# Kernel optimization log

Hardware: AMD Instinct MI355X
Metric: run time of the kernel (lower is better)

Reference implementation:

```python
import jax, jax.numpy as jnp
import numpy as np

SIZE = 1024
CODE_DIM = 256
B, H, W = 32, 32, 32


def setup_inputs() -> dict:
    key = jax.random.key(0)
    k1, k2 = jax.random.split(key)
    z = jax.random.normal(k1, (B, CODE_DIM, H, W), dtype=jnp.float32)
    embeddings = jax.random.normal(k2, (SIZE, CODE_DIM), dtype=jnp.float32)
    return {"z": z, "embeddings": embeddings}


def reference(z, embeddings):
    b, c, h, w = z.shape  # c == code_dim
    # (b, h, w, c) -> (N, c)
    flat = jnp.transpose(z, (0, 2, 3, 1)).reshape(-1, c)
    d = (
        jnp.sum(flat * flat, axis=-1, keepdims=True)
        - 2.0 * (flat @ embeddings.T)
        + jnp.sum(embeddings * embeddings, axis=-1)
    )
    idx = jnp.argmin(d, axis=-1)  # (N,)
    quantized = embeddings[idx].reshape(b, h, w, c)
    quantized = jnp.transpose(quantized, (0, 3, 1, 2))  # (b, c, h, w)
    straight_through = jax.lax.stop_gradient(quantized - z) + z
    return quantized, straight_through, idx.reshape(b, h, w)
```

## Files before the change

### kernel.cpp

```cpp
#include <hip/hip_runtime.h>

#define NPTS   32768
#define NCODES 1024
#define DIM    256
#define HWSZ   1024
#define CHW    (DIM*HWSZ)
#define QSZ    8388608

typedef __attribute__((ext_vector_type(8))) short short8;
typedef __attribute__((ext_vector_type(4))) float f32x4;

__device__ __forceinline__ void gload16(const void* g, void* l) {
    __builtin_amdgcn_global_load_lds((const __attribute__((address_space(1))) void*)g,
                                     (__attribute__((address_space(3))) void*)l,
                                     16, 0, 0);
}

__device__ __forceinline__ unsigned bf16_rne(float f) {
    unsigned u = __float_as_uint(f);
    return (u + 0x7fffu + ((u >> 16) & 1u)) >> 16;
}

__global__ void k_prep(const float* __restrict__ z, const float* __restrict__ emb,
                       short* __restrict__ Xh, short* __restrict__ Xl,
                       short* __restrict__ Eh, short* __restrict__ El,
                       float* __restrict__ e2) {
    int tid = threadIdx.x;
    if (blockIdx.x >= 1024) {
        int lane = tid & 63, w = tid >> 6;
        int k = (blockIdx.x - 1024) * 4 + w;
        const float4 v = *reinterpret_cast<const float4*>(emb + k * DIM + lane * 4);
        float f[4] = {v.x, v.y, v.z, v.w};
        short h[4], l[4];
        double s = 0.0;
        #pragma unroll
        for (int i = 0; i < 4; ++i) {
            unsigned hb = bf16_rne(f[i]);
            float hf = __uint_as_float(hb << 16);
            h[i] = (short)hb;
            l[i] = (short)bf16_rne(f[i] - hf);
            s += (double)f[i] * f[i];
        }
        *reinterpret_cast<short4*>(Eh + k * DIM + lane * 4) = make_short4(h[0], h[1], h[2], h[3]);
        *reinterpret_cast<short4*>(El + k * DIM + lane * 4) = make_short4(l[0], l[1], l[2], l[3]);
        #pragma unroll
        for (int m = 32; m >= 1; m >>= 1) s += __shfl_xor(s, m);
        if (lane == 0) e2[k] = (float)s;
        return;
    }
    __shared__ float T[64][33];
    int blk = blockIdx.x;
    int b  = blk >> 5;
    int ht = blk & 31;
    int hw0 = ht * 32;
    int n0  = b * HWSZ + hw0;
    int hq = tid & 7, cr = tid >> 3;
    int wp = tid >> 3, wc = tid & 7;
    const float* zp = z + b * CHW;
    #pragma unroll
    for (int cc = 0; cc < 4; ++cc) {
        int c0 = cc * 64;
        if (cc) __syncthreads();
        #pragma unroll
        for (int p = 0; p < 2; ++p) {
            int c = p * 32 + cr;
            float4 v = *reinterpret_cast<const float4*>(zp + (c0 + c) * HWSZ + hw0 + hq * 4);
            T[c][hq * 4 + 0] = v.x; T[c][hq * 4 + 1] = v.y;
            T[c][hq * 4 + 2] = v.z; T[c][hq * 4 + 3] = v.w;
        }
        __syncthreads();
        short8 hv, lv;
        #pragma unroll
        for (int k = 0; k < 8; ++k) {
            float f = T[wc * 8 + k][wp];
            unsigned hb = bf16_rne(f);
            float hf = __uint_as_float(hb << 16);
            hv[k] = (short)hb;
            lv[k] = (short)bf16_rne(f - hf);
        }
        *reinterpret_cast<short8*>(Xh + (n0 + wp) * DIM + c0 + wc * 8) = hv;
        *reinterpret_cast<short8*>(Xl + (n0 + wp) * DIM + c0 + wc * 8) = lv;
    }
}

__launch_bounds__(256, 4)
__global__ void k_dist(const short* __restrict__ Xh, const short* __restrict__ Xl,
                       const short* __restrict__ Eh, const short* __restrict__ El,
                       const float* __restrict__ e2, float* __restrict__ minv,
                       int* __restrict__ mini) {
    __shared__ __align__(16) short Ah[4096];
    __shared__ __align__(16) short Al[4096];
    __shared__ __align__(16) short Bh[4096];
    __shared__ __align__(16) short Bl[4096];
    __shared__ float sv[2][128];
    __shared__ int   si[2][128];

    const int tid = threadIdx.x;
    const int pt = blockIdx.x & 255;
    const int ct = blockIdx.x >> 8;
    const int n0 = pt * 128;
    const int c0 = ct * 128;

    const int w = tid >> 6, lane = tid & 63;
    const int wr = w >> 1, wc = w & 1;
    const int m16 = lane & 15, quad = lane >> 4;

    f32x4 acc[4][4];
    #pragma unroll
    for (int i = 0; i < 4; ++i)
        #pragma unroll
        for (int j = 0; j < 4; ++j) acc[i][j] = (f32x4){0.f, 0.f, 0.f, 0.f};

    const int r   = lane >> 2;
    const int swz = (((lane & 3) - ((lane >> 3) & 3)) & 3) * 8;
    const int ldsoff0 = (w * 16) * 64;
    const int ldsoff1 = (64 + w * 16) * 64;
    const int arow0 = (n0 + w * 16 + r) * DIM;
    const int arow1 = (n0 + 64 + w * 16 + r) * DIM;
    const int brow0 = (c0 + w * 16 + r) * DIM;
    const int brow1 = (c0 + 64 + w * 16 + r) * DIM;

    const int pq = ((quad + (m16 >> 1)) & 3) * 8;

    for (int t = 0; t < 8; ++t) {
        const int koff = t * 32 + swz;
        __syncthreads();
        gload16(Xh + arow0 + koff, (char*)Ah + ldsoff0);
        gload16(Xh + arow1 + koff, (char*)Ah + ldsoff1);
        gload16(Xl + arow0 + koff, (char*)Al + ldsoff0);
        gload16(Xl + arow1 + koff, (char*)Al + ldsoff1);
        gload16(Eh + brow0 + koff, (char*)Bh + ldsoff0);
        gload16(Eh + brow1 + koff, (char*)Bh + ldsoff1);
        gload16(El + brow0 + koff, (char*)Bl + ldsoff0);
        gload16(El + brow1 + koff, (char*)Bl + ldsoff1);
        __syncthreads();

        short8 ah[4], al[4], bh[4], bl[4];
        #pragma unroll
        for (int i = 0; i < 4; ++i) {
            int ar = (wr * 64 + i * 16 + m16) * 32 + pq;
            ah[i] = *(const short8*)&Ah[ar];
            al[i] = *(const short8*)&Al[ar];
        }
        #pragma unroll
        for (int j = 0; j < 4; ++j) {
            int br = (wc * 64 + j * 16 + m16) * 32 + pq;
            bh[j] = *(const short8*)&Bh[br];
            bl[j] = *(const short8*)&Bl[br];
        }
        #pragma unroll
        for (int i = 0; i < 4; ++i)
            #pragma unroll
            for (int j = 0; j < 4; ++j)
                acc[i][j] = __builtin_amdgcn_mfma_f32_16x16x32_bf16(ah[i], bh[j], acc[i][j], 0, 0, 0);
        #pragma unroll
        for (int i = 0; i < 4; ++i)
            #pragma unroll
            for (int j = 0; j < 4; ++j)
                acc[i][j] = __builtin_amdgcn_mfma_f32_16x16x32_bf16(al[i], bh[j], acc[i][j], 0, 0, 0);
        #pragma unroll
        for (int i = 0; i < 4; ++i)
            #pragma unroll
            for (int j = 0; j < 4; ++j)
                acc[i][j] = __builtin_amdgcn_mfma_f32_16x16x32_bf16(ah[i], bl[j], acc[i][j], 0, 0, 0);
    }

    float ecol[4];
    #pragma unroll
    for (int j = 0; j < 4; ++j) ecol[j] = e2[c0 + wc * 64 + j * 16 + m16];

    #pragma unroll
    for (int i = 0; i < 4; ++i) {
        #pragma unroll
        for (int rr = 0; rr < 4; ++rr) {
            float best = 3.4e38f; int bi = 0;
            #pragma unroll
            for (int j = 0; j < 4; ++j) {
                float d = fmaf(-2.f, acc[i][j][rr], ecol[j]);
                int code = c0 + wc * 64 + j * 16 + m16;
                if (d < best) { best = d; bi = code; }
            }
            #pragma unroll
            for (int m = 1; m < 16; m <<= 1) {
                float ov = __shfl_xor(best, m);
                int   oi = __shfl_xor(bi, m);
                if (ov < best || (ov == best && oi < bi)) { best = ov; bi = oi; }
            }
            if (m16 == 0) {
                int p = wr * 64 + i * 16 + quad * 4 + rr;
                sv[wc][p] = best; si[wc][p] = bi;
            }
        }
    }
    __syncthreads();
    if (tid < 128) {
        float v0 = sv[0][tid]; int i0 = si[0][tid];
        float v1 = sv[1][tid]; int i1 = si[1][tid];
        if (v1 < v0) { v0 = v1; i0 = i1; }
        minv[ct * NPTS + n0 + tid] = v0;
        mini[ct * NPTS + n0 + tid] = i0;
    }
}

__global__ void k_out(const float* __restrict__ z, const float* __restrict__ emb,
                      const float* __restrict__ minv, const int* __restrict__ mini,
                      float* __restrict__ out) {
    __shared__ float Q[32][257];
    __shared__ int sbi[32];
    int n0 = blockIdx.x * 32;
    int tid = threadIdx.x;
    if (tid < 32) {
        int n = n0 + tid;
        float bv = minv[n]; int bi = mini[n];
        #pragma unroll
        for (int g = 1; g < 8; ++g) {
            float v = minv[g * NPTS + n]; int ii = mini[g * NPTS + n];
            if (v < bv) { bv = v; bi = ii; }
        }
        sbi[tid] = bi;
        out[2 * QSZ + n] = (float)bi;
    }
    __syncthreads();
    {
        int pt = tid >> 3, co = tid & 7;
        const float* ep = emb + sbi[pt] * DIM;
        #pragma unroll
        for (int j = 0; j < 8; ++j) {
            int c = j * 32 + co * 4;
            float4 v = *reinterpret_cast<const float4*>(ep + c);
            Q[pt][c] = v.x; Q[pt][c + 1] = v.y; Q[pt][c + 2] = v.z; Q[pt][c + 3] = v.w;
        }
    }
    __syncthreads();
    int hq = tid & 7, cr = tid >> 3;
    int b = n0 >> 10, hw0 = (n0 & 1023) + hq * 4;
    #pragma unroll
    for (int it = 0; it < 8; ++it) {
        int c = it * 32 + cr;
        int off = b * CHW + c * HWSZ + hw0;
        float4 zv = *reinterpret_cast<const float4*>(z + off);
        float4 q = make_float4(Q[hq * 4 + 0][c], Q[hq * 4 + 1][c],
                               Q[hq * 4 + 2][c], Q[hq * 4 + 3][c]);
        *reinterpret_cast<float4*>(out + off) = q;
        float4 st = make_float4((q.x - zv.x) + zv.x, (q.y - zv.y) + zv.y,
                                (q.z - zv.z) + zv.z, (q.w - zv.w) + zv.w);
        *reinterpret_cast<float4*>(out + QSZ + off) = st;
    }
}

extern "C" void kernel_launch(void* const* d_in, const int* in_sizes, int n_in,
                              void* d_out, int out_size, void* d_ws, size_t ws_size,
                              hipStream_t stream) {
    const float* z   = (const float*)d_in[0];
    const float* emb = (const float*)d_in[1];
    float* out = (float*)d_out;
    float* ws  = (float*)d_ws;

    short* Eh   = (short*)ws;
    short* El   = (short*)(ws + 131072);
    float* e2   = ws + 262144;
    float* minv = ws + 263168;
    int*   mini = (int*)(ws + 525312);

    short* Xh = (short*)out;
    short* Xl = (short*)(out + 4194304);

    hipLaunchKernelGGL(k_prep, dim3(1280), dim3(256), 0, stream, z, emb, Xh, Xl, Eh, El, e2);
    hipLaunchKernelGGL(k_dist, dim3(2048), dim3(256), 0, stream, Xh, Xl, Eh, El, e2, minv, mini);
    hipLaunchKernelGGL(k_out,  dim3(1024), dim3(256), 0, stream, z, emb, minv, mini, out);
}
```

Baseline: 165.8 us.

## Double-buffer LDS tiles in distance GEMM to overlap global loads with MFMA

The k_dist main loop now uses two LDS buffers per operand and issues the global-to-LDS loads two K-steps ahead. It synchronises with explicit vmcnt/lgkmcnt waits and raw barriers instead of two __syncthreads per step. Wave priority is raised around the MFMA block. The aim is to hide global load latency behind matrix math, at the cost of doubled LDS use (launch bounds drop from 4 to 2 blocks per CU) and so lower occupancy.

```diff
diff --git a/kernel.cpp b/kernel.cpp
--- a/kernel.cpp
+++ b/kernel.cpp
@@ -83,15 +83,15 @@
     }
 }
 
-__launch_bounds__(256, 4)
+__launch_bounds__(256, 2)
 __global__ void k_dist(const short* __restrict__ Xh, const short* __restrict__ Xl,
                        const short* __restrict__ Eh, const short* __restrict__ El,
                        const float* __restrict__ e2, float* __restrict__ minv,
                        int* __restrict__ mini) {
-    __shared__ __align__(16) short Ah[4096];
-    __shared__ __align__(16) short Al[4096];
-    __shared__ __align__(16) short Bh[4096];
-    __shared__ __align__(16) short Bl[4096];
+    __shared__ __align__(16) short Ah[2][4096];
+    __shared__ __align__(16) short Al[2][4096];
+    __shared__ __align__(16) short Bh[2][4096];
+    __shared__ __align__(16) short Bl[2][4096];
     __shared__ float sv[2][128];
     __shared__ int   si[2][128];
 
@@ -122,32 +122,51 @@
 
     const int pq = ((quad + (m16 >> 1)) & 3) * 8;
 
+    #define STAGE(buf, t) do {                                        \
+        const int koff_ = (t) * 32 + swz;                             \
+        gload16(Xh + arow0 + koff_, (char*)Ah[buf] + ldsoff0);        \
+        gload16(Xh + arow1 + koff_, (char*)Ah[buf] + ldsoff1);        \
+        gload16(Xl + arow0 + koff_, (char*)Al[buf] + ldsoff0);        \
+        gload16(Xl + arow1 + koff_, (char*)Al[buf] + ldsoff1);        \
+        gload16(Eh + brow0 + koff_, (char*)Bh[buf] + ldsoff0);        \
+        gload16(Eh + brow1 + koff_, (char*)Bh[buf] + ldsoff1);        \
+        gload16(El + brow0 + koff_, (char*)Bl[buf] + ldsoff0);        \
+        gload16(El + brow1 + koff_, (char*)Bl[buf] + ldsoff1);        \
+    } while (0)
+
+    STAGE(0, 0);
+    STAGE(1, 1);
+
+    #pragma unroll
     for (int t = 0; t < 8; ++t) {
-        const int koff = t * 32 + swz;
-        __syncthreads();
-        gload16(Xh + arow0 + koff, (char*)Ah + ldsoff0);
-        gload16(Xh + arow1 + koff, (char*)Ah + ldsoff1);
-        gload16(Xl + arow0 + koff, (char*)Al + ldsoff0);
-        gload16(Xl + arow1 + koff, (char*)Al + ldsoff1);
-        gload16(Eh + brow0 + koff, (char*)Bh + ldsoff0);
-        gload16(Eh + brow1 + koff, (char*)Bh + ldsoff1);
-        gload16(El + brow0 + koff, (char*)Bl + ldsoff0);
-        gload16(El + brow1 + koff, (char*)Bl + ldsoff1);
-        __syncthreads();
+        const int cur = t & 1;
+        if (t < 7) asm volatile("s_waitcnt vmcnt(8)" ::: "memory");
+        else       asm volatile("s_waitcnt vmcnt(0)" ::: "memory");
+        __builtin_amdgcn_s_barrier();
 
         short8 ah[4], al[4], bh[4], bl[4];
+        const short* Ahc = Ah[cur]; const short* Alc = Al[cur];
+        const short* Bhc = Bh[cur]; const short* Blc = Bl[cur];
         #pragma unroll
         for (int i = 0; i < 4; ++i) {
             int ar = (wr * 64 + i * 16 + m16) * 32 + pq;
-            ah[i] = *(const short8*)&Ah[ar];
-            al[i] = *(const short8*)&Al[ar];
+            ah[i] = *(const short8*)&Ahc[ar];
+            al[i] = *(const short8*)&Alc[ar];
         }
         #pragma unroll
         for (int j = 0; j < 4; ++j) {
             int br = (wc * 64 + j * 16 + m16) * 32 + pq;
-            bh[j] = *(const short8*)&Bh[br];
-            bl[j] = *(const short8*)&Bl[br];
-        }
+            bh[j] = *(const short8*)&Bhc[br];
+            bl[j] = *(const short8*)&Blc[br];
+        }
+        asm volatile("s_waitcnt lgkmcnt(0)" ::: "memory");
+        __builtin_amdgcn_sched_barrier(0);
+        __builtin_amdgcn_s_barrier();
+
+        if (t < 6) STAGE(cur, t + 2);
+        __builtin_amdgcn_sched_barrier(0);
+
+        __builtin_amdgcn_s_setprio(1);
         #pragma unroll
         for (int i = 0; i < 4; ++i)
             #pragma unroll
@@ -163,7 +182,10 @@
             #pragma unroll
             for (int j = 0; j < 4; ++j)
                 acc[i][j] = __builtin_amdgcn_mfma_f32_16x16x32_bf16(ah[i], bl[j], acc[i][j], 0, 0, 0);
-    }
+        __builtin_amdgcn_s_setprio(0);
+        __builtin_amdgcn_sched_barrier(0);
+    }
+    #undef STAGE
 
     float ecol[4];
     #pragma unroll
```

Measured after the change: 179.3 us. 8.1% more time.

## Load MFMA operands directly from global memory, dropping LDS staging

Applied to the files above, without the earlier changes.

Removes the shared-memory staging of the bf16 hi/lo operand tiles. Each wave now loads its MFMA fragments straight from global memory into registers, with the k-loop fully unrolled and no block barriers. The block-index mapping is reordered so the eight code tiles for one point tile run adjacently, which should help L2 reuse of the X rows. MFMA sections are wrapped in s_setprio and launch bounds are relaxed to 3 waves per SIMD. Each wave now reads data that other waves in the block also read, so more cache traffic and register pressure are the trade-off for removing barrier and LDS costs.

```diff
diff --git a/kernel.cpp b/kernel.cpp
--- a/kernel.cpp
+++ b/kernel.cpp
@@ -9,12 +9,6 @@
 
 typedef __attribute__((ext_vector_type(8))) short short8;
 typedef __attribute__((ext_vector_type(4))) float f32x4;
-
-__device__ __forceinline__ void gload16(const void* g, void* l) {
-    __builtin_amdgcn_global_load_lds((const __attribute__((address_space(1))) void*)g,
-                                     (__attribute__((address_space(3))) void*)l,
-                                     16, 0, 0);
-}
 
 __device__ __forceinline__ unsigned bf16_rne(float f) {
     unsigned u = __float_as_uint(f);
@@ -83,21 +77,17 @@
     }
 }
 
-__launch_bounds__(256, 4)
+__launch_bounds__(256, 3)
 __global__ void k_dist(const short* __restrict__ Xh, const short* __restrict__ Xl,
                        const short* __restrict__ Eh, const short* __restrict__ El,
                        const float* __restrict__ e2, float* __restrict__ minv,
                        int* __restrict__ mini) {
-    __shared__ __align__(16) short Ah[4096];
-    __shared__ __align__(16) short Al[4096];
-    __shared__ __align__(16) short Bh[4096];
-    __shared__ __align__(16) short Bl[4096];
     __shared__ float sv[2][128];
     __shared__ int   si[2][128];
 
     const int tid = threadIdx.x;
-    const int pt = blockIdx.x & 255;
-    const int ct = blockIdx.x >> 8;
+    const int pt = blockIdx.x >> 3;
+    const int ct = blockIdx.x & 7;
     const int n0 = pt * 128;
     const int c0 = ct * 128;
 
@@ -111,43 +101,24 @@
         #pragma unroll
         for (int j = 0; j < 4; ++j) acc[i][j] = (f32x4){0.f, 0.f, 0.f, 0.f};
 
-    const int r   = lane >> 2;
-    const int swz = (((lane & 3) - ((lane >> 3) & 3)) & 3) * 8;
-    const int ldsoff0 = (w * 16) * 64;
-    const int ldsoff1 = (64 + w * 16) * 64;
-    const int arow0 = (n0 + w * 16 + r) * DIM;
-    const int arow1 = (n0 + 64 + w * 16 + r) * DIM;
-    const int brow0 = (c0 + w * 16 + r) * DIM;
-    const int brow1 = (c0 + 64 + w * 16 + r) * DIM;
-
-    const int pq = ((quad + (m16 >> 1)) & 3) * 8;
-
+    const int abase = (n0 + wr * 64 + m16) * DIM + quad * 8;
+    const int bbase = (c0 + wc * 64 + m16) * DIM + quad * 8;
+
+    #pragma unroll
     for (int t = 0; t < 8; ++t) {
-        const int koff = t * 32 + swz;
-        __syncthreads();
-        gload16(Xh + arow0 + koff, (char*)Ah + ldsoff0);
-        gload16(Xh + arow1 + koff, (char*)Ah + ldsoff1);
-        gload16(Xl + arow0 + koff, (char*)Al + ldsoff0);
-        gload16(Xl + arow1 + koff, (char*)Al + ldsoff1);
-        gload16(Eh + brow0 + koff, (char*)Bh + ldsoff0);
-        gload16(Eh + brow1 + koff, (char*)Bh + ldsoff1);
-        gload16(El + brow0 + koff, (char*)Bl + ldsoff0);
-        gload16(El + brow1 + koff, (char*)Bl + ldsoff1);
-        __syncthreads();
-
+        const int ko = t * 32;
         short8 ah[4], al[4], bh[4], bl[4];
         #pragma unroll
         for (int i = 0; i < 4; ++i) {
-            int ar = (wr * 64 + i * 16 + m16) * 32 + pq;
-            ah[i] = *(const short8*)&Ah[ar];
-            al[i] = *(const short8*)&Al[ar];
+            ah[i] = *reinterpret_cast<const short8*>(Xh + abase + i * 16 * DIM + ko);
+            al[i] = *reinterpret_cast<const short8*>(Xl + abase + i * 16 * DIM + ko);
         }
         #pragma unroll
         for (int j = 0; j < 4; ++j) {
-            int br = (wc * 64 + j * 16 + m16) * 32 + pq;
-            bh[j] = *(const short8*)&Bh[br];
-            bl[j] = *(const short8*)&Bl[br];
-        }
+            bh[j] = *reinterpret_cast<const short8*>(Eh + bbase + j * 16 * DIM + ko);
+            bl[j] = *reinterpret_cast<const short8*>(El + bbase + j * 16 * DIM + ko);
+        }
+        __builtin_amdgcn_s_setprio(1);
         #pragma unroll
         for (int i = 0; i < 4; ++i)
             #pragma unroll
@@ -163,6 +134,7 @@
             #pragma unroll
             for (int j = 0; j < 4; ++j)
                 acc[i][j] = __builtin_amdgcn_mfma_f32_16x16x32_bf16(ah[i], bl[j], acc[i][j], 0, 0, 0);
+        __builtin_amdgcn_s_setprio(0);
     }
 
     float ecol[4];
```

New measurement: 231.3 us. +39.5%, slower.

## Fuse z transpose and bf16 split into distance kernel A-operand loads

Applied to the files above, without the earlier changes.

The prep kernel no longer transposes z and writes hi/lo bf16 copies to global memory. The distance kernel now reads z in its original NCHW layout straight into registers, splits each value into bf16 hi/lo parts in-register, and feeds them to MFMA, dropping the A tiles from LDS. This removes one full pass over z and the write and re-read of the Xh/Xl intermediates. In exchange, each of the 8 column tiles re-reads and re-converts the same z data using strided scalar loads. It also adds register pressure, so launch bounds drop to 3 waves.

```diff
diff --git a/kernel.cpp b/kernel.cpp
--- a/kernel.cpp
+++ b/kernel.cpp
@@ -21,75 +21,36 @@
     return (u + 0x7fffu + ((u >> 16) & 1u)) >> 16;
 }
 
-__global__ void k_prep(const float* __restrict__ z, const float* __restrict__ emb,
-                       short* __restrict__ Xh, short* __restrict__ Xl,
+__global__ void k_prep(const float* __restrict__ emb,
                        short* __restrict__ Eh, short* __restrict__ El,
                        float* __restrict__ e2) {
     int tid = threadIdx.x;
-    if (blockIdx.x >= 1024) {
-        int lane = tid & 63, w = tid >> 6;
-        int k = (blockIdx.x - 1024) * 4 + w;
-        const float4 v = *reinterpret_cast<const float4*>(emb + k * DIM + lane * 4);
-        float f[4] = {v.x, v.y, v.z, v.w};
-        short h[4], l[4];
-        double s = 0.0;
-        #pragma unroll
-        for (int i = 0; i < 4; ++i) {
-            unsigned hb = bf16_rne(f[i]);
-            float hf = __uint_as_float(hb << 16);
-            h[i] = (short)hb;
-            l[i] = (short)bf16_rne(f[i] - hf);
-            s += (double)f[i] * f[i];
-        }
-        *reinterpret_cast<short4*>(Eh + k * DIM + lane * 4) = make_short4(h[0], h[1], h[2], h[3]);
-        *reinterpret_cast<short4*>(El + k * DIM + lane * 4) = make_short4(l[0], l[1], l[2], l[3]);
-        #pragma unroll
-        for (int m = 32; m >= 1; m >>= 1) s += __shfl_xor(s, m);
-        if (lane == 0) e2[k] = (float)s;
-        return;
-    }
-    __shared__ float T[64][33];
-    int blk = blockIdx.x;
-    int b  = blk >> 5;
-    int ht = blk & 31;
-    int hw0 = ht * 32;
-    int n0  = b * HWSZ + hw0;
-    int hq = tid & 7, cr = tid >> 3;
-    int wp = tid >> 3, wc = tid & 7;
-    const float* zp = z + b * CHW;
-    #pragma unroll
-    for (int cc = 0; cc < 4; ++cc) {
-        int c0 = cc * 64;
-        if (cc) __syncthreads();
-        #pragma unroll
-        for (int p = 0; p < 2; ++p) {
-            int c = p * 32 + cr;
-            float4 v = *reinterpret_cast<const float4*>(zp + (c0 + c) * HWSZ + hw0 + hq * 4);
-            T[c][hq * 4 + 0] = v.x; T[c][hq * 4 + 1] = v.y;
-            T[c][hq * 4 + 2] = v.z; T[c][hq * 4 + 3] = v.w;
-        }
-        __syncthreads();
-        short8 hv, lv;
-        #pragma unroll
-        for (int k = 0; k < 8; ++k) {
-            float f = T[wc * 8 + k][wp];
-            unsigned hb = bf16_rne(f);
-            float hf = __uint_as_float(hb << 16);
-            hv[k] = (short)hb;
-            lv[k] = (short)bf16_rne(f - hf);
-        }
-        *reinterpret_cast<short8*>(Xh + (n0 + wp) * DIM + c0 + wc * 8) = hv;
-        *reinterpret_cast<short8*>(Xl + (n0 + wp) * DIM + c0 + wc * 8) = lv;
-    }
-}
-
-__launch_bounds__(256, 4)
-__global__ void k_dist(const short* __restrict__ Xh, const short* __restrict__ Xl,
+    int lane = tid & 63, w = tid >> 6;
+    int k = blockIdx.x * 4 + w;
+    const float4 v = *reinterpret_cast<const float4*>(emb + k * DIM + lane * 4);
+    float f[4] = {v.x, v.y, v.z, v.w};
+    short h[4], l[4];
+    double s = 0.0;
+    #pragma unroll
+    for (int i = 0; i < 4; ++i) {
+        unsigned hb = bf16_rne(f[i]);
+        float hf = __uint_as_float(hb << 16);
+        h[i] = (short)hb;
+        l[i] = (short)bf16_rne(f[i] - hf);
+        s += (double)f[i] * f[i];
+    }
+    *reinterpret_cast<short4*>(Eh + k * DIM + lane * 4) = make_short4(h[0], h[1], h[2], h[3]);
+    *reinterpret_cast<short4*>(El + k * DIM + lane * 4) = make_short4(l[0], l[1], l[2], l[3]);
+    #pragma unroll
+    for (int m = 32; m >= 1; m >>= 1) s += __shfl_xor(s, m);
+    if (lane == 0) e2[k] = (float)s;
+}
+
+__launch_bounds__(256, 3)
+__global__ void k_dist(const float* __restrict__ z,
                        const short* __restrict__ Eh, const short* __restrict__ El,
                        const float* __restrict__ e2, float* __restrict__ minv,
                        int* __restrict__ mini) {
-    __shared__ __align__(16) short Ah[4096];
-    __shared__ __align__(16) short Al[4096];
     __shared__ __align__(16) short Bh[4096];
     __shared__ __align__(16) short Bl[4096];
     __shared__ float sv[2][128];
@@ -115,33 +76,43 @@
     const int swz = (((lane & 3) - ((lane >> 3) & 3)) & 3) * 8;
     const int ldsoff0 = (w * 16) * 64;
     const int ldsoff1 = (64 + w * 16) * 64;
-    const int arow0 = (n0 + w * 16 + r) * DIM;
-    const int arow1 = (n0 + 64 + w * 16 + r) * DIM;
     const int brow0 = (c0 + w * 16 + r) * DIM;
     const int brow1 = (c0 + 64 + w * 16 + r) * DIM;
-
     const int pq = ((quad + (m16 >> 1)) & 3) * 8;
+
+    const int bb  = n0 >> 10;
+    const int hwb = (n0 & 1023) + wr * 64 + m16;
+    const float* zl = z + bb * CHW + (quad * 8) * HWSZ + hwb;
 
     for (int t = 0; t < 8; ++t) {
         const int koff = t * 32 + swz;
         __syncthreads();
-        gload16(Xh + arow0 + koff, (char*)Ah + ldsoff0);
-        gload16(Xh + arow1 + koff, (char*)Ah + ldsoff1);
-        gload16(Xl + arow0 + koff, (char*)Al + ldsoff0);
-        gload16(Xl + arow1 + koff, (char*)Al + ldsoff1);
         gload16(Eh + brow0 + koff, (char*)Bh + ldsoff0);
         gload16(Eh + brow1 + koff, (char*)Bh + ldsoff1);
         gload16(El + brow0 + koff, (char*)Bl + ldsoff0);
         gload16(El + brow1 + koff, (char*)Bl + ldsoff1);
+
+        short8 ah[4], al[4];
+        #pragma unroll
+        for (int i = 0; i < 4; ++i) {
+            float f[8];
+            #pragma unroll
+            for (int e = 0; e < 8; ++e)
+                f[e] = zl[(t * 32 + e) * HWSZ + i * 16];
+            short8 hv, lv;
+            #pragma unroll
+            for (int e = 0; e < 8; ++e) {
+                unsigned hb = bf16_rne(f[e]);
+                float hf = __uint_as_float(hb << 16);
+                hv[e] = (short)hb;
+                lv[e] = (short)bf16_rne(f[e] - hf);
+            }
+            ah[i] = hv; al[i] = lv;
+        }
+
         __syncthreads();
 
-        short8 ah[4], al[4], bh[4], bl[4];
-        #pragma unroll
-        for (int i = 0; i < 4; ++i) {
-            int ar = (wr * 64 + i * 16 + m16) * 32 + pq;
-            ah[i] = *(const short8*)&Ah[ar];
-            al[i] = *(const short8*)&Al[ar];
-        }
+        short8 bh[4], bl[4];
         #pragma unroll
         for (int j = 0; j < 4; ++j) {
             int br = (wc * 64 + j * 16 + m16) * 32 + pq;
@@ -262,10 +233,7 @@
     float* minv = ws + 263168;
     int*   mini = (int*)(ws + 525312);
 
-    short* Xh = (short*)out;
-    short* Xl = (short*)(out + 4194304);
-
-    hipLaunchKernelGGL(k_prep, dim3(1280), dim3(256), 0, stream, z, emb, Xh, Xl, Eh, El, e2);
-    hipLaunchKernelGGL(k_dist, dim3(2048), dim3(256), 0, stream, Xh, Xl, Eh, El, e2, minv, mini);
+    hipLaunchKernelGGL(k_prep, dim3(256),  dim3(256), 0, stream, emb, Eh, El, e2);
+    hipLaunchKernelGGL(k_dist, dim3(2048), dim3(256), 0, stream, z, Eh, El, e2, minv, mini);
     hipLaunchKernelGGL(k_out,  dim3(1024), dim3(256), 0, stream, z, emb, minv, mini, out);
 }
```

New measurement: 172.6 us. +4.1%, slower.
